# Kernel tuning notes

Hardware: AMD Instinct MI355X
Metric: run time of the kernel (lower is better)

Reference implementation:

```python
import jax, jax.numpy as jnp
import numpy as np

W = 5   # window_size
H = 8   # num_heads


def setup_inputs() -> dict:
    key = jax.random.key(0)
    ks = jax.random.split(key, 8)
    B, L, D, nC = 32, 2048, 1024, 2
    s = 0.02
    return {
        "x": jax.random.normal(ks[0], (B, L, D), jnp.float32),
        "in_proj_w": jax.random.normal(ks[1], (3 * D, D), jnp.float32) * s,
        "in_proj_b": jnp.zeros((3 * D,), jnp.float32),
        "out_proj_w": jax.random.normal(ks[2], (D, D), jnp.float32) * s,
        "out_proj_b": jnp.zeros((D,), jnp.float32),
        "out_w": jax.random.normal(ks[3], (nC, D), jnp.float32) * s,
        "out_b": jnp.zeros((nC,), jnp.float32),
        "x_len": jax.random.randint(ks[4], (32,), 1, L + 1, dtype=jnp.int32),
    }


def reference(x, in_proj_w, in_proj_b, out_proj_w, out_proj_b, out_w, out_b, x_len):
    # x: (B, L, D). Dropout layers are identity (eval mode). x_len is unused
    # by the original forward as well.
    B, L, D = x.shape
    nC = out_w.shape[0]
    hd = D // H
    T = 2 * W + 1  # context length per window = 11

    # pad end of time axis by W, as in F.pad(x, (0,0,0,window_size))
    xp = jnp.pad(x, ((0, 0), (0, W), (0, 0)))

    # loop frames f = W, 2W, ... < L; window covers [f-W, f+W], write at f-W
    starts = np.arange(0, L - W, W)               # (Nw,) static
    idx = starts[:, None] + np.arange(T)          # (Nw, T)
    ctx = xp[:, idx, :]                           # (B, Nw, T, D)
    Nw = starts.shape[0]

    wq, wk, wv = jnp.split(in_proj_w, 3, axis=0)
    bq, bk, bv = jnp.split(in_proj_b, 3)

    # only the center token's attention output is kept -> query center only
    q = ctx[:, :, W, :] @ wq.T + bq               # (B, Nw, D)
    k = ctx @ wk.T + bk                           # (B, Nw, T, D)
    v = ctx @ wv.T + bv                           # (B, Nw, T, D)

    q = q.reshape(B, Nw, H, hd)
    k = k.reshape(B, Nw, T, H, hd)
    v = v.reshape(B, Nw, T, H, hd)

    scale = float(1.0 / np.sqrt(hd))
    scores = jnp.einsum('bnhd,bnthd->bnht', q, k) * scale
    attn = jax.nn.softmax(scores, axis=-1)        # (B, Nw, H, T)
    o = jnp.einsum('bnht,bnthd->bnhd', attn, v).reshape(B, Nw, D)
    feat = o @ out_proj_w.T + out_proj_b          # (B, Nw, D)
    probs = feat @ out_w.T + out_b                # (B, Nw, nC)

    # non-window frames stay zero -> log_softmax of zeros = log(1/nC)
    final = jnp.zeros((B, L, nC), x.dtype).at[:, starts, :].set(probs)
    return jax.nn.log_softmax(final.reshape(-1, nC), axis=1)
```

## Files before the change

### kernel.cpp

```cpp
#include <hip/hip_runtime.h>

#define B_  32
#define L_  2048
#define D_  1024
#define NW_ 409
#define W_  5
#define T_  11
#define H_  8
#define HD_ 128
#define MQ  (B_*NW_)
#define MQP 13184

typedef __attribute__((ext_vector_type(16))) float f32x16;
typedef __attribute__((ext_vector_type(4)))  float f32x4;
typedef __attribute__((ext_vector_type(8))) __bf16 bf16x8;

__device__ __forceinline__ float b2f(unsigned short u) {
  union { unsigned int i; float f; } x; x.i = ((unsigned int)u) << 16; return x.f;
}
__device__ __forceinline__ unsigned short f2b(float f) {
  union { float f; unsigned int i; } x; x.f = f;
  unsigned int r = (x.i + 0x7FFFu + ((x.i >> 16) & 1u)) >> 16;
  return (unsigned short)r;
}
__device__ __forceinline__ float2 bf2x(unsigned int u) {
  union { unsigned int i; float f; } lo, hi;
  lo.i = u << 16; hi.i = u & 0xffff0000u;
  return make_float2(lo.f, hi.f);
}

__device__ __forceinline__ void async_copy16(const void* g, void* l) {
  __builtin_amdgcn_global_load_lds(
      (const __attribute__((address_space(1))) void*)g,
      (__attribute__((address_space(3))) void*)l, 16, 0, 0);
}

__device__ __forceinline__ float dot8(uint4 a, uint4 b) {
  float2 x, y; float s = 0.f;
  x = bf2x(a.x); y = bf2x(b.x); s += x.x * y.x + x.y * y.y;
  x = bf2x(a.y); y = bf2x(b.y); s += x.x * y.x + x.y * y.y;
  x = bf2x(a.z); y = bf2x(b.z); s += x.x * y.x + x.y * y.y;
  x = bf2x(a.w); y = bf2x(b.w); s += x.x * y.x + x.y * y.y;
  return s;
}

__device__ __forceinline__ void cvt_body(const float* __restrict__ in,
                                         unsigned short* __restrict__ out,
                                         int i0, int stride, int n4) {
  for (int i = i0; i < n4; i += stride) {
    float4 v = ((const float4*)in)[i];
    ushort4 o;
    o.x = f2b(v.x); o.y = f2b(v.y); o.z = f2b(v.z); o.w = f2b(v.w);
    ((ushort4*)out)[i] = o;
  }
}
__global__ __launch_bounds__(256)
void mega1_kernel(const float* __restrict__ x, unsigned short* __restrict__ xb,
                  const float* __restrict__ ipw, unsigned short* __restrict__ win,
                  const float* __restrict__ ow, const float* __restrict__ opw,
                  float* __restrict__ Wcp, float* __restrict__ out) {
  const int blk = blockIdx.x, tid = threadIdx.x;
  if (blk < 2048) {
    cvt_body(x, xb, blk * 256 + tid, 2048 * 256, 16777216);
  } else if (blk < 2304) {
    cvt_body(ipw, win, (blk - 2048) * 256 + tid, 256 * 256, 786432);
  } else if (blk < 2816) {
    out[(blk - 2304) * 256 + tid] = -0.69314718055994531f;
  } else {
    int bb = blk - 2816;
    int eb = bb >> 3, seg = bb & 7;
    int d = seg * 256 + tid;
    int c = d >> 10, dd = d & 1023;
    float acc = 0.f;
    int e0 = eb * 64;
#pragma unroll 8
    for (int e = e0; e < e0 + 64; e++) acc += ow[c * D_ + e] * opw[e * D_ + dd];
    Wcp[eb * 2048 + d] = acc;
  }
}

__global__ void wc_reduce_kernel(const float* __restrict__ Wcp,
                                 const float* __restrict__ ow, const float* __restrict__ opb,
                                 const float* __restrict__ ob,
                                 float* __restrict__ Wc, float* __restrict__ bc) {
  int d = blockIdx.x * 256 + threadIdx.x;
  float s = 0.f;
#pragma unroll
  for (int eb = 0; eb < 16; eb++) s += Wcp[eb * 2048 + d];
  Wc[d] = s;
  if (blockIdx.x == 0 && threadIdx.x < 128) {
    int c = threadIdx.x >> 6, lane = threadIdx.x & 63;
    float p = 0.f;
#pragma unroll
    for (int j = 0; j < 16; j++) p += ow[c * D_ + lane + 64 * j] * opb[lane + 64 * j];
#pragma unroll
    for (int off = 32; off > 0; off >>= 1) p += __shfl_down(p, off);
    if (lane == 0) bc[c] = p + ob[c];
  }
}

__global__ __launch_bounds__(256)
void wvh_kernel(const float* __restrict__ Wcp, const float* __restrict__ ipw,
                const float* __restrict__ ipb, float* __restrict__ bc,
                unsigned short* __restrict__ WvHb) {
  const int c = blockIdx.x >> 3, h = blockIdx.x & 7;
  const int tid = threadIdx.x;
  __shared__ float wcs[128];
  if (tid < 128) {
    float s = 0.f;
#pragma unroll
    for (int eb = 0; eb < 16; eb++) s += Wcp[eb * 2048 + c * 1024 + h * 128 + tid];
    wcs[tid] = s;
  }
  __syncthreads();
  const float* wv = ipw + 2048 * 1024;
#pragma unroll
  for (int j = 0; j < 4; j++) {
    int e = j * 256 + tid;
    float acc = 0.f;
    for (int dd = 0; dd < 128; dd++)
      acc += wcs[dd] * wv[(size_t)(h * 128 + dd) * 1024 + e];
    WvHb[(c * 8 + h) * 1024 + e] = f2b(acc);
  }
  if (tid == 0) {
    float gb = 0.f;
    for (int dd = 0; dd < 128; dd++) gb += wcs[dd] * ipb[2048 + h * 128 + dd];
    atomicAdd(&bc[c], gb);
  }
}

__global__ __launch_bounds__(256)
void gk_kernel(const unsigned short* __restrict__ xb,
               const unsigned short* __restrict__ WvHb,
               float* __restrict__ G) {
  const int wave = threadIdx.x >> 6, lane = threadIdx.x & 63;
  const int r0 = (blockIdx.x * 4 + wave) * 16;
  const int l15 = lane & 15, kh = lane >> 4;
  const unsigned short* ap = xb + (size_t)(r0 + l15) * 1024 + kh * 8;
  const unsigned short* bp = WvHb + l15 * 1024 + kh * 8;
  f32x4 acc = (f32x4)0.0f;
  for (int kt = 0; kt < 1024; kt += 32) {
    bf16x8 a = *(const bf16x8*)(ap + kt);
    bf16x8 b = *(const bf16x8*)(bp + kt);
    acc = __builtin_amdgcn_mfma_f32_16x16x32_bf16(a, b, acc, 0, 0, 0);
  }
#pragma unroll
  for (int r = 0; r < 4; r++)
    G[(size_t)(r0 + kh * 4 + r) * 16 + l15] = acc[r];
}

template<bool GATHER>
__global__ __launch_bounds__(256)
void gemm_bt_kernel(const unsigned short* __restrict__ A,
                    const unsigned short* __restrict__ Bw,
                    unsigned short* __restrict__ C,
                    const float* __restrict__ bias,
                    int N, int K) {
  __shared__ __align__(16) unsigned short sA[128 * 64];
  __shared__ __align__(16) unsigned short sB[128 * 64];
  const int h = blockIdx.y * gridDim.x + blockIdx.x;
  const int chunk = (gridDim.x * gridDim.y) >> 3;
  const int lg = (h & 7) * chunk + (h >> 3);
  const int bx = lg % gridDim.x, by = lg / gridDim.x;
  const int tid = threadIdx.x;
  const int row0 = by * 128;
  const int col0 = bx * 128;
  const int wave = tid >> 6, lane = tid & 63;
  const int wm = wave & 1, wn = wave >> 1;
  const int l31 = lane & 31, lh = lane >> 5;

  const unsigned short* Asrc[4];
  const unsigned short* Bsrc[4];
#pragma unroll
  for (int u = 0; u < 4; u++) {
    int c = tid + 256 * u;
    int r = c >> 3, kc = ((c & 7) - r) & 7;
    Bsrc[u] = Bw + (size_t)(col0 + r) * K + kc * 8;
    size_t arow;
    if constexpr (GATHER) {
      int mm = row0 + r;
      if (mm >= MQ) mm = 0;
      int b = mm / NW_, n = mm - b * NW_;
      arow = (size_t)b * L_ + (size_t)(W_ * n + W_);
    } else {
      arow = (size_t)(row0 + r);
    }
    Asrc[u] = A + arow * K + kc * 8;
  }

  int offA[4][2], offB[4][2];
#pragma unroll
  for (int kc = 0; kc < 4; kc++) {
    int c8 = kc * 2 + lh;
#pragma unroll
    for (int i = 0; i < 2; i++) {
      int rb = wn * 64 + i * 32 + l31;
      offB[kc][i] = (rb * 8 + ((c8 + rb) & 7)) * 8;
      int ra = wm * 64 + i * 32 + l31;
      offA[kc][i] = (ra * 8 + ((c8 + ra) & 7)) * 8;
    }
  }

  f32x16 acc[2][2];
#pragma unroll
  for (int i = 0; i < 2; i++)
#pragma unroll
    for (int j = 0; j < 2; j++) acc[i][j] = (f32x16)0.0f;

  for (int kt = 0; kt < K; kt += 64) {
#pragma unroll
    for (int u = 0; u < 4; u++)
      async_copy16(Asrc[u] + kt, &sA[(tid + 256 * u) * 8]);
#pragma unroll
    for (int u = 0; u < 4; u++)
      async_copy16(Bsrc[u] + kt, &sB[(tid + 256 * u) * 8]);
    __syncthreads();
#pragma unroll
    for (int kc = 0; kc < 4; kc++) {
      bf16x8 a0 = *(const bf16x8*)&sA[offA[kc][0]];
      bf16x8 a1 = *(const bf16x8*)&sA[offA[kc][1]];
      bf16x8 b0 = *(const bf16x8*)&sB[offB[kc][0]];
      bf16x8 b1 = *(const bf16x8*)&sB[offB[kc][1]];
      acc[0][0] = __builtin_amdgcn_mfma_f32_32x32x16_bf16(a0, b0, acc[0][0], 0, 0, 0);
      acc[0][1] = __builtin_amdgcn_mfma_f32_32x32x16_bf16(a0, b1, acc[0][1], 0, 0, 0);
      acc[1][0] = __builtin_amdgcn_mfma_f32_32x32x16_bf16(a1, b0, acc[1][0], 0, 0, 0);
      acc[1][1] = __builtin_amdgcn_mfma_f32_32x32x16_bf16(a1, b1, acc[1][1], 0, 0, 0);
    }
    __syncthreads();
  }

#pragma unroll
  for (int i = 0; i < 2; i++) {
#pragma unroll
    for (int j = 0; j < 2; j++) {
      int gc = col0 + wn * 64 + j * 32 + l31;
      float bv = bias ? bias[gc] : 0.0f;
#pragma unroll
      for (int r = 0; r < 16; r++) {
        int gr = row0 + wm * 64 + i * 32 + (r & 3) + 8 * (r >> 2) + 4 * lh;
        C[(size_t)gr * N + gc] = f2b(acc[i][j][r] + bv);
      }
    }
  }
}

__global__ __launch_bounds__(256)
void attn_kernel(const unsigned short* __restrict__ q,
                 const unsigned short* __restrict__ kb,
                 const float* __restrict__ G, const float* __restrict__ bc,
                 float* __restrict__ out) {
  const int g = blockIdx.x;
  const int xcd = g & 7, idx = g >> 3;
  const int logical = (xcd < 4) ? (xcd * 205 + idx)
                                : (820 + (xcd - 4) * 204 + idx);
  const int wave = threadIdx.x >> 6, lane = threadIdx.x & 63;
  const int p = logical * 4 + wave;
  const int m0 = 2 * p, m1 = m0 + 1;
  const int b0 = m0 / NW_, n0 = m0 - b0 * NW_;
  const int b1 = m1 / NW_, n1 = m1 - b1 * NW_;
  const bool adj = (n0 != NW_ - 1);
  const size_t rb0 = (size_t)b0 * L_ * 1024;
  const size_t rb1 = (size_t)b1 * L_ * 1024;
  const int d0 = lane * 16;

  const unsigned short* qp0 = q + (size_t)m0 * D_ + d0;
  uint4 qa0 = *(const uint4*)qp0, qa1 = *(const uint4*)(qp0 + 8);
  const unsigned short* qp1 = q + (size_t)m1 * D_ + d0;
  uint4 qb0 = *(const uint4*)qp1, qb1 = *(const uint4*)(qp1 + 8);

  float svA[T_], svB[T_];
#pragma unroll
  for (int t = 0; t < T_ + W_; t++) {
    uint4 k0, k1;
    bool liveA = false;
    if (t < T_) {
      int posA = W_ * n0 + t;
      float sc = 0.f;
      if (posA < L_) {
        const unsigned short* kr = kb + rb0 + (size_t)posA * 1024 + d0;
        k0 = *(const uint4*)kr; k1 = *(const uint4*)(kr + 8);
        liveA = true;
        sc = dot8(qa0, k0) + dot8(qa1, k1);
      }
      sc += __shfl_xor(sc, 1);
      sc += __shfl_xor(sc, 2);
      sc += __shfl_xor(sc, 4);
      svA[t] = sc * 0.08838834764831845f;
    }
    if (t >= W_) {
      int tb = t - W_;
      int posB = W_ * n1 + tb;
      float sc = 0.f;
      if (posB < L_) {
        uint4 j0, j1;
        if (adj && liveA) { j0 = k0; j1 = k1; }
        else {
          const unsigned short* kr = kb + rb1 + (size_t)posB * 1024 + d0;
          j0 = *(const uint4*)kr; j1 = *(const uint4*)(kr + 8);
        }
        sc = dot8(qb0, j0) + dot8(qb1, j1);
      }
      sc += __shfl_xor(sc, 1);
      sc += __shfl_xor(sc, 2);
      sc += __shfl_xor(sc, 4);
      svB[tb] = sc * 0.08838834764831845f;
    }
  }

  {
    float mx = svA[0];
#pragma unroll
    for (int t = 1; t < T_; t++) mx = fmaxf(mx, svA[t]);
    float sum = 0.f;
#pragma unroll
    for (int t = 0; t < T_; t++) { svA[t] = expf(svA[t] - mx); sum += svA[t]; }
    float inv = 1.f / sum;
#pragma unroll
    for (int t = 0; t < T_; t++) svA[t] *= inv;
  }
  {
    float mx = svB[0];
#pragma unroll
    for (int t = 1; t < T_; t++) mx = fmaxf(mx, svB[t]);
    float sum = 0.f;
#pragma unroll
    for (int t = 0; t < T_; t++) { svB[t] = expf(svB[t] - mx); sum += svB[t]; }
    float inv = 1.f / sum;
#pragma unroll
    for (int t = 0; t < T_; t++) svB[t] *= inv;
  }

  float pA0 = 0.f, pA1 = 0.f, pB0 = 0.f, pB1 = 0.f;
  {
    const int s = lane & 7, hh = lane >> 3;
#pragma unroll
    for (int rep = 0; rep < 2; rep++) {
      int t = s + 8 * rep;
      if (t < T_) {
        int posA = W_ * n0 + t;
        if (posA < L_) {
          const float* ga = G + ((size_t)b0 * L_ + posA) * 16 + hh;
          pA0 += svA[t] * ga[0];
          pA1 += svA[t] * ga[8];
        }
        int posB = W_ * n1 + t;
        if (posB < L_) {
          const float* gb = G + ((size_t)b1 * L_ + posB) * 16 + hh;
          pB0 += svB[t] * gb[0];
          pB1 += svB[t] * gb[8];
        }
      }
    }
  }
#pragma unroll
  for (int off = 32; off > 0; off >>= 1) {
    pA0 += __shfl_down(pA0, off);
    pA1 += __shfl_down(pA1, off);
    pB0 += __shfl_down(pB0, off);
    pB1 += __shfl_down(pB1, off);
  }

  if (lane == 0) {
    {
      float s0 = pA0 + bc[0], s1 = pA1 + bc[1];
      float smx = fmaxf(s0, s1);
      float lse = smx + logf(expf(s0 - smx) + expf(s1 - smx));
      size_t row = (size_t)b0 * L_ + (size_t)(W_ * n0);
      out[row * 2 + 0] = s0 - lse;
      out[row * 2 + 1] = s1 - lse;
    }
    {
      float s0 = pB0 + bc[0], s1 = pB1 + bc[1];
      float smx = fmaxf(s0, s1);
      float lse = smx + logf(expf(s0 - smx) + expf(s1 - smx));
      size_t row = (size_t)b1 * L_ + (size_t)(W_ * n1);
      out[row * 2 + 0] = s0 - lse;
      out[row * 2 + 1] = s1 - lse;
    }
  }
}

extern "C" void kernel_launch(void* const* d_in, const int* in_sizes, int n_in,
                              void* d_out, int out_size, void* d_ws, size_t ws_size,
                              hipStream_t stream) {
  const float* x          = (const float*)d_in[0];
  const float* in_proj_w  = (const float*)d_in[1];
  const float* in_proj_b  = (const float*)d_in[2];
  const float* out_proj_w = (const float*)d_in[3];
  const float* out_proj_b = (const float*)d_in[4];
  const float* out_w      = (const float*)d_in[5];
  const float* out_b      = (const float*)d_in[6];
  float* out = (float*)d_out;

  char* ws = (char*)d_ws;
  unsigned short* qout = (unsigned short*)(ws);
  unsigned short* win  = (unsigned short*)(ws + 33554432);
  float*          Wc   = (float*)(ws + 41943040);
  float*          bc   = (float*)(ws + 41951232);
  float*          Wcp  = (float*)(ws + 41959424);
  unsigned short* WvHb = (unsigned short*)(ws + 42090496);
  unsigned short* xb   = (unsigned short*)(ws + 50331648);
  unsigned short* kb   = (unsigned short*)(ws + 184549376);
  float*          G    = (float*)(ws + 318767104);

  mega1_kernel<<<2944, 256, 0, stream>>>(x, xb, in_proj_w, win,
                                         out_w, out_proj_w, Wcp, out);
  wc_reduce_kernel<<<8, 256, 0, stream>>>(Wcp, out_w, out_proj_b, out_b, Wc, bc);
  wvh_kernel<<<16, 256, 0, stream>>>(Wcp, in_proj_w, in_proj_b, bc, WvHb);

  dim3 gk(8, 512);
  gemm_bt_kernel<false><<<gk, 256, 0, stream>>>(xb, win + 1048576, kb,
                                                in_proj_b + 1024, 1024, 1024);
  dim3 gq(8, 103);
  gemm_bt_kernel<true><<<gq, 256, 0, stream>>>(xb, win, qout, in_proj_b, 1024, 1024);

  gk_kernel<<<1024, 256, 0, stream>>>(xb, WvHb, G);

  attn_kernel<<<1636, 256, 0, stream>>>(qout, kb, G, bc, out);
}
```

Measured before the change: 717.2 us.

## Fuse K-projection, Q-gather GEMM and G kernel into one launch; widen wvh grid

Merges the two projection GEMM launches and the G (x·WvH) kernel into one kernel whose block index range picks which body to run. This removes two launch boundaries and lets the small gk tail overlap with the GEMM blocks instead of running after them. The wvh kernel is also split four ways over output columns, going from 16 to 64 blocks, so it parallelises better. In exchange every block reserves GEMM-sized shared memory even on the gk path, and the bias pointer is now dereferenced unconditionally.

```diff
diff --git a/kernel.cpp b/kernel.cpp
--- a/kernel.cpp
+++ b/kernel.cpp
@@ -103,7 +103,7 @@
 void wvh_kernel(const float* __restrict__ Wcp, const float* __restrict__ ipw,
                 const float* __restrict__ ipb, float* __restrict__ bc,
                 unsigned short* __restrict__ WvHb) {
-  const int c = blockIdx.x >> 3, h = blockIdx.x & 7;
+  const int c = blockIdx.x >> 5, h = (blockIdx.x >> 2) & 7, j = blockIdx.x & 3;
   const int tid = threadIdx.x;
   __shared__ float wcs[128];
   if (tid < 128) {
@@ -114,54 +114,29 @@
   }
   __syncthreads();
   const float* wv = ipw + 2048 * 1024;
-#pragma unroll
-  for (int j = 0; j < 4; j++) {
+  {
     int e = j * 256 + tid;
     float acc = 0.f;
     for (int dd = 0; dd < 128; dd++)
       acc += wcs[dd] * wv[(size_t)(h * 128 + dd) * 1024 + e];
     WvHb[(c * 8 + h) * 1024 + e] = f2b(acc);
   }
-  if (tid == 0) {
+  if (j == 0 && tid == 0) {
     float gb = 0.f;
     for (int dd = 0; dd < 128; dd++) gb += wcs[dd] * ipb[2048 + h * 128 + dd];
     atomicAdd(&bc[c], gb);
   }
 }
 
-__global__ __launch_bounds__(256)
-void gk_kernel(const unsigned short* __restrict__ xb,
-               const unsigned short* __restrict__ WvHb,
-               float* __restrict__ G) {
-  const int wave = threadIdx.x >> 6, lane = threadIdx.x & 63;
-  const int r0 = (blockIdx.x * 4 + wave) * 16;
-  const int l15 = lane & 15, kh = lane >> 4;
-  const unsigned short* ap = xb + (size_t)(r0 + l15) * 1024 + kh * 8;
-  const unsigned short* bp = WvHb + l15 * 1024 + kh * 8;
-  f32x4 acc = (f32x4)0.0f;
-  for (int kt = 0; kt < 1024; kt += 32) {
-    bf16x8 a = *(const bf16x8*)(ap + kt);
-    bf16x8 b = *(const bf16x8*)(bp + kt);
-    acc = __builtin_amdgcn_mfma_f32_16x16x32_bf16(a, b, acc, 0, 0, 0);
-  }
-#pragma unroll
-  for (int r = 0; r < 4; r++)
-    G[(size_t)(r0 + kh * 4 + r) * 16 + l15] = acc[r];
-}
-
 template<bool GATHER>
-__global__ __launch_bounds__(256)
-void gemm_bt_kernel(const unsigned short* __restrict__ A,
-                    const unsigned short* __restrict__ Bw,
-                    unsigned short* __restrict__ C,
-                    const float* __restrict__ bias,
-                    int N, int K) {
-  __shared__ __align__(16) unsigned short sA[128 * 64];
-  __shared__ __align__(16) unsigned short sB[128 * 64];
-  const int h = blockIdx.y * gridDim.x + blockIdx.x;
-  const int chunk = (gridDim.x * gridDim.y) >> 3;
+__device__ void gemm_body(const unsigned short* __restrict__ A,
+                          const unsigned short* __restrict__ Bw,
+                          unsigned short* __restrict__ C,
+                          const float* __restrict__ bias,
+                          int N, int K, int h, int gx, int chunk,
+                          unsigned short* sA, unsigned short* sB) {
   const int lg = (h & 7) * chunk + (h >> 3);
-  const int bx = lg % gridDim.x, by = lg / gridDim.x;
+  const int bx = lg % gx, by = lg / gx;
   const int tid = threadIdx.x;
   const int row0 = by * 128;
   const int col0 = bx * 128;
@@ -234,13 +209,54 @@
 #pragma unroll
     for (int j = 0; j < 2; j++) {
       int gc = col0 + wn * 64 + j * 32 + l31;
-      float bv = bias ? bias[gc] : 0.0f;
+      float bv = bias[gc];
 #pragma unroll
       for (int r = 0; r < 16; r++) {
         int gr = row0 + wm * 64 + i * 32 + (r & 3) + 8 * (r >> 2) + 4 * lh;
         C[(size_t)gr * N + gc] = f2b(acc[i][j][r] + bv);
       }
     }
+  }
+}
+
+__device__ void gk_body(const unsigned short* __restrict__ xb,
+                        const unsigned short* __restrict__ WvHb,
+                        float* __restrict__ G, int blk) {
+  const int wave = threadIdx.x >> 6, lane = threadIdx.x & 63;
+  const int r0 = (blk * 4 + wave) * 16;
+  const int l15 = lane & 15, kh = lane >> 4;
+  const unsigned short* ap = xb + (size_t)(r0 + l15) * 1024 + kh * 8;
+  const unsigned short* bp = WvHb + l15 * 1024 + kh * 8;
+  f32x4 acc = (f32x4)0.0f;
+  for (int kt = 0; kt < 1024; kt += 32) {
+    bf16x8 a = *(const bf16x8*)(ap + kt);
+    bf16x8 b = *(const bf16x8*)(bp + kt);
+    acc = __builtin_amdgcn_mfma_f32_16x16x32_bf16(a, b, acc, 0, 0, 0);
+  }
+#pragma unroll
+  for (int r = 0; r < 4; r++)
+    G[(size_t)(r0 + kh * 4 + r) * 16 + l15] = acc[r];
+}
+
+__global__ __launch_bounds__(256)
+void fused_main_kernel(const unsigned short* __restrict__ xb,
+                       const unsigned short* __restrict__ win,
+                       const unsigned short* __restrict__ WvHb,
+                       unsigned short* __restrict__ kb,
+                       unsigned short* __restrict__ qout,
+                       float* __restrict__ G,
+                       const float* __restrict__ ipb) {
+  __shared__ __align__(16) unsigned short sA[128 * 64];
+  __shared__ __align__(16) unsigned short sB[128 * 64];
+  const int b = blockIdx.x;
+  if (b < 4096) {
+    gemm_body<false>(xb, win + 1048576, kb, ipb + 1024, 1024, 1024,
+                     b, 8, 512, sA, sB);
+  } else if (b < 4920) {
+    gemm_body<true>(xb, win, qout, ipb, 1024, 1024,
+                    b - 4096, 8, 103, sA, sB);
+  } else {
+    gk_body(xb, WvHb, G, b - 4920);
   }
 }
 
@@ -406,15 +422,10 @@
   mega1_kernel<<<2944, 256, 0, stream>>>(x, xb, in_proj_w, win,
                                          out_w, out_proj_w, Wcp, out);
   wc_reduce_kernel<<<8, 256, 0, stream>>>(Wcp, out_w, out_proj_b, out_b, Wc, bc);
-  wvh_kernel<<<16, 256, 0, stream>>>(Wcp, in_proj_w, in_proj_b, bc, WvHb);
-
-  dim3 gk(8, 512);
-  gemm_bt_kernel<false><<<gk, 256, 0, stream>>>(xb, win + 1048576, kb,
-                                                in_proj_b + 1024, 1024, 1024);
-  dim3 gq(8, 103);
-  gemm_bt_kernel<true><<<gq, 256, 0, stream>>>(xb, win, qout, in_proj_b, 1024, 1024);
-
-  gk_kernel<<<1024, 256, 0, stream>>>(xb, WvHb, G);
+  wvh_kernel<<<64, 256, 0, stream>>>(Wcp, in_proj_w, in_proj_b, bc, WvHb);
+
+  fused_main_kernel<<<5944, 256, 0, stream>>>(xb, win, WvHb, kb, qout, G,
+                                              in_proj_b);
 
   attn_kernel<<<1636, 256, 0, stream>>>(qout, kb, G, bc, out);
 }
```

Result: faster. 680.6 us (-5.1%).
